# Optimization experiments

Measured on AMD Instinct MI355X. Metric: run time of the kernel, lower is better.

Reference implementation:

```python
import jax, jax.numpy as jnp
import numpy as np

D = 1024          # d_model
H = 16            # num_attention_heads
HD = D // H       # head_dim
WIN = 512         # attention_window (total)
W = WIN // 2      # one-sided window
S = 4096          # seq_len
B = 2             # batch
NEG = jnp.finfo(jnp.float32).min


def setup_inputs() -> dict:
    key = jax.random.key(0)
    ks = jax.random.split(key, 9)
    sc = 0.02
    return {
        "query": jax.random.normal(ks[0], (S, B, D), dtype=jnp.float32),
        "Wq": jax.random.normal(ks[1], (D, D), dtype=jnp.float32) * sc,
        "bq": jnp.zeros((D,), dtype=jnp.float32),
        "Wk": jax.random.normal(ks[2], (D, D), dtype=jnp.float32) * sc,
        "bk": jnp.zeros((D,), dtype=jnp.float32),
        "Wv": jax.random.normal(ks[3], (D, D), dtype=jnp.float32) * sc,
        "bv": jnp.zeros((D,), dtype=jnp.float32),
        "Wo": jax.random.normal(ks[4], (D, D), dtype=jnp.float32) * sc,
        "bo": jnp.zeros((D,), dtype=jnp.float32),
    }


def _heads(x):  # [B,S,D] -> [B,H,S,HD]
    b, s, _ = x.shape
    return x.reshape(b, s, H, HD).transpose(0, 2, 1, 3)


def reference(query, Wq, bq, Wk, bk, Wv, bv, Wo, bo):
    s, b, d = query.shape
    x = query.transpose(1, 0, 2)                       # [B,S,D]
    q = _heads(x @ Wq + bq) / jnp.sqrt(jnp.float32(HD))  # [B,H,S,HD]
    k = _heads(x @ Wk + bk)
    v = _heads(x @ Wv + bv)

    nc = s // W                                        # number of chunks
    # pad keys/values with one window of zeros on each side of seq axis
    kp = jnp.pad(k, ((0, 0), (0, 0), (W, W), (0, 0)))  # [B,H,S+2W,HD]
    vp = jnp.pad(v, ((0, 0), (0, 0), (W, W), (0, 0)))
    idx = jnp.arange(nc)[:, None] * W + jnp.arange(3 * W)[None, :]  # [nc,3W]
    kc = kp[:, :, idx]                                 # [B,H,nc,3W,HD]
    vc = vp[:, :, idx]
    qc = q.reshape(b, H, nc, W, HD)                    # [B,H,nc,W,HD]

    scores = jnp.einsum("bhcrd,bhckd->bhcrk", qc, kc)  # [B,H,nc,W,3W]

    r = jnp.arange(W)[:, None]                         # query offset in chunk
    kk = jnp.arange(3 * W)[None, :]
    band = (kk >= r) & (kk <= r + 2 * W)               # |kpos-qpos| <= W
    kpos = jnp.arange(nc)[:, None, None] * W + kk[None] - W   # [nc,1,3W] global key pos
    mask = band[None] & (kpos >= 0) & (kpos < s)       # [nc,W,3W]

    scores = jnp.where(mask[None, None], scores, NEG)
    probs = jax.nn.softmax(scores, axis=-1)
    out = jnp.einsum("bhcrk,bhckd->bhcrd", probs, vc)  # [B,H,nc,W,HD]
    out = out.reshape(b, H, s, HD).transpose(0, 2, 1, 3).reshape(b, s, d)
    out = out.transpose(1, 0, 2)                       # [S,B,D]
    return out @ Wo + bo
```

## Files before the change

### kernel.cpp

```cpp
#include <hip/hip_runtime.h>
#include <hip/hip_bf16.h>

#define SEQ 4096
#define BATCH 2
#define DMODEL 1024
#define NH 16
#define HDIM 64
#define NEGM (-1.0e30f)
#define NT 16

typedef __attribute__((ext_vector_type(8))) short bf16x8;
typedef __attribute__((ext_vector_type(8))) unsigned short us8;
typedef __attribute__((ext_vector_type(4))) unsigned short us4;
typedef __attribute__((ext_vector_type(4))) float f32x4;

__device__ __forceinline__ unsigned short f2bf(float f) {
    union { float f; unsigned u; } v; v.f = f;
    unsigned u = v.u;
    return (unsigned short)((u + 0x7fffu + ((u >> 16) & 1u)) >> 16);
}

#define GL16(g, l)                                                              \
    __builtin_amdgcn_global_load_lds(                                           \
        (const __attribute__((address_space(1))) unsigned int*)(g),             \
        (__attribute__((address_space(3))) unsigned int*)(l), 16, 0, 0)

__global__ __launch_bounds__(256) void transpose_w(const float* __restrict__ W,
                                                   unsigned short* __restrict__ Wt,
                                                   float scale) {
    __shared__ float tile[64][65];
    const int n0 = blockIdx.x * 64, k0 = blockIdx.y * 64;
    const int tx = threadIdx.x;
    for (int dy = threadIdx.y; dy < 64; dy += 4)
        tile[dy][tx] = W[(size_t)(k0 + dy) * DMODEL + n0 + tx];
    __syncthreads();
    for (int dy = threadIdx.y; dy < 64; dy += 4)
        Wt[(size_t)(n0 + dy) * DMODEL + k0 + tx] = f2bf(tile[tx][dy] * scale);
}

__global__ __launch_bounds__(256) void build_bcat(const float* __restrict__ bq,
                                                  const float* __restrict__ bk,
                                                  const float* __restrict__ bv,
                                                  float* __restrict__ bcat) {
    int i = blockIdx.x * 256 + threadIdx.x;
    float v;
    if (i < 1024) v = bq[i] * 0.125f;
    else if (i < 2048) v = bk[i - 1024];
    else v = bv[i - 2048];
    bcat[i] = v;
}

__global__ __launch_bounds__(256) void convert_x(const float* __restrict__ q,
                                                 unsigned short* __restrict__ xb) {
    int t = blockIdx.x * 256 + threadIdx.x;
    int d4 = (t & 255) * 4;
    int row = t >> 8;
    int b = row >> 12, s = row & (SEQ - 1);
    float4 v = *(const float4*)(q + ((size_t)s * BATCH + b) * DMODEL + d4);
    us4 o;
    o[0] = f2bf(v.x); o[1] = f2bf(v.y); o[2] = f2bf(v.z); o[3] = f2bf(v.w);
    *(us4*)(xb + (size_t)row * DMODEL + d4) = o;
}

__device__ __forceinline__ void store_qkv(float v0, float v1, float v2, float v3,
                                          int row0, int col, float bval,
                                          unsigned short* __restrict__ qb,
                                          unsigned short* __restrict__ kb,
                                          unsigned short* __restrict__ vtb) {
    const int proj = col >> 10;
    const int ch = col & 1023;
    const int h = ch >> 6, hd = ch & 63;
    float vv[4] = {v0, v1, v2, v3};
    if (proj == 2) {
        const int b = row0 >> 12, s = row0 & (SEQ - 1);
        us4 o;
#pragma unroll
        for (int r = 0; r < 4; ++r) o[r] = f2bf(vv[r] + bval);
        *(us4*)(vtb + ((size_t)(b * NH + h) * HDIM + hd) * SEQ + s) = o;
    } else {
        unsigned short* dst = (proj == 0) ? qb : kb;
#pragma unroll
        for (int r = 0; r < 4; ++r) {
            const int row = row0 + r;
            const int b = row >> 12, s = row & (SEQ - 1);
            dst[((size_t)(b * NH + h) * SEQ + s) * HDIM + hd] = f2bf(vv[r] + bval);
        }
    }
}

__global__ __launch_bounds__(512) void gemm192(const unsigned short* __restrict__ A,
                                               const unsigned short* __restrict__ Bt,
                                               const float* __restrict__ bias,
                                               unsigned short* __restrict__ qb,
                                               unsigned short* __restrict__ kb,
                                               unsigned short* __restrict__ vtb) {
    __shared__ __align__(16) unsigned short lds[57344];
    const int tid = threadIdx.x;
    const int lane = tid & 63, wid = tid >> 6;
    const int lr = lane & 15, lg = lane >> 4;
    const int wm = wid >> 2, wn = wid & 3;
    const int cpx = (int)gridDim.x >> 3;
    const int orig = ((int)blockIdx.x & 7) * cpx + ((int)blockIdx.x >> 3);
    const int m0 = (orig >> 4) * 256;
    const int n0 = (orig & 15) * 192;

    const int srow = wid * 8 + (lane >> 3);
    const int scol = ((lane & 7) ^ (lane >> 3)) << 3;

    f32x4 acc[8][3];
#pragma unroll
    for (int m = 0; m < 8; ++m)
#pragma unroll
        for (int n = 0; n < 3; ++n) {
            f32x4 z = {0.f, 0.f, 0.f, 0.f};
            acc[m][n] = z;
        }

    const unsigned short* gA = A + (size_t)(m0 + srow) * DMODEL + scol;
    const unsigned short* gB = Bt + (size_t)(n0 + srow) * DMODEL + scol;

#define STAGE192(kt, bsel)                                                       \
    do {                                                                         \
        const unsigned short* ga_ = gA + (kt) * 64;                              \
        unsigned short* la_ = &lds[(bsel) * 28672 + wid * 512];                  \
        _Pragma("unroll")                                                        \
        for (int r_ = 0; r_ < 4; ++r_)                                           \
            GL16(ga_ + (size_t)r_ * 64 * DMODEL, la_ + r_ * 4096);               \
        const unsigned short* gb_ = gB + (kt) * 64;                              \
        unsigned short* lb_ = &lds[(bsel) * 28672 + 16384 + wid * 512];          \
        _Pragma("unroll")                                                        \
        for (int r_ = 0; r_ < 3; ++r_)                                           \
            GL16(gb_ + (size_t)r_ * 64 * DMODEL, lb_ + r_ * 4096);               \
    } while (0)

    STAGE192(0, 0);
    asm volatile("s_waitcnt vmcnt(0)" ::: "memory");
    __builtin_amdgcn_s_barrier();
    asm volatile("" ::: "memory");

    const int swz = (lr & 7) << 3;
    for (int t = 0; t < NT; ++t) {
        if (t + 1 < NT) STAGE192(t + 1, (t + 1) & 1);
        const unsigned short* Ab = &lds[(t & 1) * 28672];
        const unsigned short* Bb = Ab + 16384;
#pragma unroll
        for (int ks = 0; ks < 2; ++ks) {
            const int kc = (ks * 32 + lg * 8) ^ swz;
            bf16x8 af[8], bfr[3];
#pragma unroll
            for (int fm = 0; fm < 8; ++fm)
                af[fm] = *(const bf16x8*)&Ab[(wm * 128 + fm * 16 + lr) * 64 + kc];
#pragma unroll
            for (int fn = 0; fn < 3; ++fn)
                bfr[fn] = *(const bf16x8*)&Bb[(wn * 48 + fn * 16 + lr) * 64 + kc];
            __builtin_amdgcn_s_setprio(1);
#pragma unroll
            for (int fm = 0; fm < 8; ++fm)
#pragma unroll
                for (int fn = 0; fn < 3; ++fn)
                    acc[fm][fn] = __builtin_amdgcn_mfma_f32_16x16x32_bf16(af[fm], bfr[fn], acc[fm][fn], 0, 0, 0);
            __builtin_amdgcn_s_setprio(0);
        }
        __builtin_amdgcn_sched_barrier(0);
        asm volatile("s_waitcnt lgkmcnt(0)" ::: "memory");
        asm volatile("s_waitcnt vmcnt(0)" ::: "memory");
        __builtin_amdgcn_s_barrier();
        asm volatile("" ::: "memory");
    }
#undef STAGE192

#pragma unroll
    for (int fn = 0; fn < 3; ++fn) {
        const int col = n0 + wn * 48 + fn * 16 + lr;
        const float bval = bias[col];
#pragma unroll
        for (int fm = 0; fm < 8; ++fm) {
            const int row0 = m0 + wm * 128 + fm * 16 + lg * 4;
            store_qkv(acc[fm][fn][0], acc[fm][fn][1], acc[fm][fn][2], acc[fm][fn][3],
                      row0, col, bval, qb, kb, vtb);
        }
    }
}

__global__ __launch_bounds__(512) void gemm256o(const unsigned short* __restrict__ A,
                                                const unsigned short* __restrict__ Bt,
                                                const float* __restrict__ bias,
                                                float* __restrict__ out) {
    __shared__ __align__(16) unsigned short lds[73728];
    const int tid = threadIdx.x;
    const int lane = tid & 63, wid = tid >> 6;
    const int lr = lane & 15, lg = lane >> 4;
    const int wm = wid >> 1, wn = wid & 1;
    const int cpx = (int)gridDim.x >> 3;
    const int orig = ((int)blockIdx.x & 7) * cpx + ((int)blockIdx.x >> 3);
    const int m0 = (orig >> 3) * 256;
    const int n0 = (orig & 7) * 128;

    const int srow = wid * 8 + (lane >> 3);
    const int scol = ((lane & 7) ^ (lane >> 3)) << 3;

    f32x4 acc[4][4];
#pragma unroll
    for (int m = 0; m < 4; ++m)
#pragma unroll
        for (int n = 0; n < 4; ++n) {
            f32x4 z = {0.f, 0.f, 0.f, 0.f};
            acc[m][n] = z;
        }

    const unsigned short* gA = A + (size_t)(m0 + srow) * DMODEL + scol;
    const unsigned short* gB = Bt + (size_t)(n0 + srow) * DMODEL + scol;

#define STAGE_A(kt, bsel)                                                        \
    do {                                                                         \
        const unsigned short* ga_ = gA + (kt) * 64;                              \
        unsigned short* la_ = &lds[(bsel) * 24576 + wid * 512];                  \
        _Pragma("unroll")                                                        \
        for (int r_ = 0; r_ < 4; ++r_)                                           \
            GL16(ga_ + (size_t)r_ * 64 * DMODEL, la_ + r_ * 4096);               \
    } while (0)
#define STAGE_B(kt, bsel)                                                        \
    do {                                                                         \
        const unsigned short* gb_ = gB + (kt) * 64;                              \
        unsigned short* lb_ = &lds[(bsel) * 24576 + 16384 + wid * 512];          \
        _Pragma("unroll")                                                        \
        for (int r_ = 0; r_ < 2; ++r_)                                           \
            GL16(gb_ + (size_t)r_ * 64 * DMODEL, lb_ + r_ * 4096);               \
    } while (0)

    STAGE_A(0, 0); STAGE_B(0, 0);
    STAGE_A(1, 1); STAGE_B(1, 1);
    asm volatile("s_waitcnt vmcnt(6)" ::: "memory");
    __builtin_amdgcn_s_barrier();
    asm volatile("" ::: "memory");

    const int swz = (lr & 7) << 3;
    int bs = 0;
    for (int t = 0; t < NT; ++t) {
        const int b2 = bs >= 1 ? bs - 1 : bs + 2;
        if (t + 2 < NT) { STAGE_A(t + 2, b2); STAGE_B(t + 2, b2); }
        const unsigned short* Ab = &lds[bs * 24576];
        const unsigned short* Bb = Ab + 16384;
#pragma unroll
        for (int ks = 0; ks < 2; ++ks) {
            const int kc = (ks * 32 + lg * 8) ^ swz;
            bf16x8 af[4], bfr[4];
#pragma unroll
            for (int fm = 0; fm < 4; ++fm)
                af[fm] = *(const bf16x8*)&Ab[(wm * 64 + fm * 16 + lr) * 64 + kc];
#pragma unroll
            for (int fn = 0; fn < 4; ++fn)
                bfr[fn] = *(const bf16x8*)&Bb[(wn * 64 + fn * 16 + lr) * 64 + kc];
            __builtin_amdgcn_s_setprio(1);
#pragma unroll
            for (int fm = 0; fm < 4; ++fm)
#pragma unroll
                for (int fn = 0; fn < 4; ++fn)
                    acc[fm][fn] = __builtin_amdgcn_mfma_f32_16x16x32_bf16(af[fm], bfr[fn], acc[fm][fn], 0, 0, 0);
            __builtin_amdgcn_s_setprio(0);
        }
        __builtin_amdgcn_sched_barrier(0);
        asm volatile("s_waitcnt lgkmcnt(0)" ::: "memory");
        if (t + 2 < NT)
            asm volatile("s_waitcnt vmcnt(6)" ::: "memory");
        else
            asm volatile("s_waitcnt vmcnt(0)" ::: "memory");
        __builtin_amdgcn_s_barrier();
        asm volatile("" ::: "memory");
        bs = bs < 2 ? bs + 1 : 0;
    }
#undef STAGE_A
#undef STAGE_B

#pragma unroll
    for (int fn = 0; fn < 4; ++fn) {
        const int col = n0 + wn * 64 + fn * 16 + lr;
        const float bval = bias[col];
#pragma unroll
        for (int fm = 0; fm < 4; ++fm) {
            const int row0 = m0 + wm * 64 + fm * 16 + lg * 4;
#pragma unroll
            for (int r = 0; r < 4; ++r) {
                const int row = row0 + r;
                const int b = row >> 12, s = row & (SEQ - 1);
                out[((size_t)s * BATCH + b) * DMODEL + col] = acc[fm][fn][r] + bval;
            }
        }
    }
}

__global__ __launch_bounds__(512) void attn_kernel(const unsigned short* __restrict__ qb,
                                                   const unsigned short* __restrict__ kb,
                                                   const unsigned short* __restrict__ vtb,
                                                   unsigned short* __restrict__ ao) {
    __shared__ __align__(16) unsigned short Ks[64][72];
    __shared__ __align__(16) unsigned short Vs[64][72];
    __shared__ __align__(16) unsigned short Ps[8][16][72];
    const int tid = threadIdx.x;
    const int lane = tid & 63, wid = tid >> 6;
    const int lr = lane & 15, lg = lane >> 4;
    const int blk = ((int)blockIdx.x & 7) * 128 + ((int)blockIdx.x >> 3);
    const int qc = blk & 31, h = (blk >> 5) & 15, b = blk >> 9;
    const int q0 = qc * 128;
    const unsigned short* Qh = qb + (size_t)(b * NH + h) * SEQ * HDIM;
    const unsigned short* Kh = kb + (size_t)(b * NH + h) * SEQ * HDIM;
    const unsigned short* Vh = vtb + (size_t)(b * NH + h) * HDIM * SEQ;
    const int qw = q0 + wid * 16;

    bf16x8 qf0 = *(const bf16x8*)(Qh + (size_t)(qw + lr) * HDIM + lg * 8);
    bf16x8 qf1 = *(const bf16x8*)(Qh + (size_t)(qw + lr) * HDIM + 32 + lg * 8);

    f32x4 oacc[4];
    float lsum[4];
#pragma unroll
    for (int n = 0; n < 4; ++n) {
        f32x4 z = {0.f, 0.f, 0.f, 0.f};
        oacc[n] = z;
    }
#pragma unroll
    for (int r = 0; r < 4; ++r) lsum[r] = 0.f;

    int lo = q0 - 256; if (lo < 0) lo = 0;
    int hi = q0 + 384; if (hi > SEQ) hi = SEQ;

    const int srow = tid >> 3, sseg = (tid & 7) * 8;

    us8 kpre = *(const us8*)(Kh + (size_t)(lo + srow) * HDIM + sseg);
    us8 vpre = *(const us8*)(Vh + (size_t)srow * SEQ + lo + sseg);

    for (int kt = lo; kt < hi; kt += 64) {
        __syncthreads();
        *(us8*)&Ks[srow][sseg] = kpre;
        *(us8*)&Vs[srow][sseg] = vpre;
        if (kt + 64 < hi) {
            kpre = *(const us8*)(Kh + (size_t)(kt + 64 + srow) * HDIM + sseg);
            vpre = *(const us8*)(Vh + (size_t)srow * SEQ + kt + 64 + sseg);
        }
        __builtin_amdgcn_sched_barrier(0);
        __syncthreads();

        f32x4 sf[4];
        __builtin_amdgcn_s_setprio(1);
#pragma unroll
        for (int n = 0; n < 4; ++n) {
            bf16x8 kf0 = *(const bf16x8*)&Ks[n * 16 + lr][lg * 8];
            bf16x8 kf1 = *(const bf16x8*)&Ks[n * 16 + lr][32 + lg * 8];
            f32x4 z = {0.f, 0.f, 0.f, 0.f};
            sf[n] = __builtin_amdgcn_mfma_f32_16x16x32_bf16(qf0, kf0, z, 0, 0, 0);
            sf[n] = __builtin_amdgcn_mfma_f32_16x16x32_bf16(qf1, kf1, sf[n], 0, 0, 0);
        }
        __builtin_amdgcn_s_setprio(0);
        const bool full = (kt >= qw - 241) && (kt + 63 <= qw + 256);
        if (!full) {
#pragma unroll
            for (int r = 0; r < 4; ++r) {
                const int qpos = qw + lg * 4 + r;
#pragma unroll
                for (int n = 0; n < 4; ++n) {
                    const int kpos = kt + n * 16 + lr;
                    if (kpos < qpos - 256 || kpos > qpos + 256) sf[n][r] = NEGM;
                }
            }
        }
#pragma unroll
        for (int n = 0; n < 4; ++n)
#pragma unroll
            for (int r = 0; r < 4; ++r) {
                const float p = __expf(sf[n][r]);
                lsum[r] += p;
                Ps[wid][lg * 4 + r][n * 16 + lr] = f2bf(p);
            }

        asm volatile("s_waitcnt lgkmcnt(0)" ::: "memory");
        __builtin_amdgcn_s_setprio(1);
#pragma unroll
        for (int ks = 0; ks < 2; ++ks) {
            bf16x8 pf = *(const bf16x8*)&Ps[wid][lr][ks * 32 + lg * 8];
#pragma unroll
            for (int n = 0; n < 4; ++n) {
                bf16x8 vf = *(const bf16x8*)&Vs[n * 16 + lr][ks * 32 + lg * 8];
                oacc[n] = __builtin_amdgcn_mfma_f32_16x16x32_bf16(pf, vf, oacc[n], 0, 0, 0);
            }
        }
        __builtin_amdgcn_s_setprio(0);
    }

#pragma unroll
    for (int d = 1; d < 16; d <<= 1)
#pragma unroll
        for (int r = 0; r < 4; ++r) lsum[r] += __shfl_xor(lsum[r], d, 64);

#pragma unroll
    for (int n = 0; n < 4; ++n)
#pragma unroll
        for (int r = 0; r < 4; ++r) {
            const int row = qw + lg * 4 + r;
            const float o = oacc[n][r] / lsum[r];
            ao[((size_t)b * SEQ + row) * DMODEL + h * HDIM + n * 16 + lr] = f2bf(o);
        }
}

extern "C" void kernel_launch(void* const* d_in, const int* in_sizes, int n_in,
                              void* d_out, int out_size, void* d_ws, size_t ws_size,
                              hipStream_t stream) {
    (void)in_sizes; (void)n_in; (void)out_size; (void)ws_size;
    const float* query = (const float*)d_in[0];
    const float* Wq = (const float*)d_in[1];
    const float* bq = (const float*)d_in[2];
    const float* Wk = (const float*)d_in[3];
    const float* bk = (const float*)d_in[4];
    const float* Wv = (const float*)d_in[5];
    const float* bv = (const float*)d_in[6];
    const float* Wo = (const float*)d_in[7];
    const float* bo = (const float*)d_in[8];
    float* out = (float*)d_out;

    char* ws = (char*)d_ws;
    unsigned short* xb   = (unsigned short*)ws;
    unsigned short* wcat = (unsigned short*)(ws + (16ull << 20));
    unsigned short* wot  = (unsigned short*)(ws + (22ull << 20));
    float*          bcat = (float*)(ws + (24ull << 20));
    unsigned short* qb   = (unsigned short*)(ws + (25ull << 20));
    unsigned short* kb   = (unsigned short*)(ws + (41ull << 20));
    unsigned short* vtb  = (unsigned short*)(ws + (57ull << 20));
    unsigned short* ao   = xb;

    transpose_w<<<dim3(16, 16), dim3(64, 4), 0, stream>>>(Wq, wcat, 0.125f);
    transpose_w<<<dim3(16, 16), dim3(64, 4), 0, stream>>>(Wk, wcat + 1024 * 1024, 1.0f);
    transpose_w<<<dim3(16, 16), dim3(64, 4), 0, stream>>>(Wv, wcat + 2 * 1024 * 1024, 1.0f);
    transpose_w<<<dim3(16, 16), dim3(64, 4), 0, stream>>>(Wo, wot, 1.0f);
    build_bcat<<<12, 256, 0, stream>>>(bq, bk, bv, bcat);
    convert_x<<<8192, 256, 0, stream>>>(query, xb);

    gemm192<<<512, 512, 0, stream>>>(xb, wcat, bcat, qb, kb, vtb);
    attn_kernel<<<1024, 512, 0, stream>>>(qb, kb, vtb, ao);
    gemm256o<<<256, 512, 0, stream>>>(ao, wot, bo, out);
}
```

Measured before the change: 169.1 us.

## Give each attention wave 32 query rows and halve the block size

The attention kernel now runs 4 waves of 256 threads, each handling two 16-row query groups instead of one. K and V fragments loaded from shared memory are reused across both groups, and each thread stages two rows of K/V per tile. This halves the LDS reads of K/V per query row and the number of waves that sync per tile. In exchange it needs more registers per wave for accumulators and has fewer waves per block to hide latency.

Result: slower. 178.8 us (+5.8%).

```diff
diff --git a/kernel.cpp b/kernel.cpp
--- a/kernel.cpp
+++ b/kernel.cpp
@@ -289,13 +289,13 @@
     }
 }
 
-__global__ __launch_bounds__(512) void attn_kernel(const unsigned short* __restrict__ qb,
+__global__ __launch_bounds__(256) void attn_kernel(const unsigned short* __restrict__ qb,
                                                    const unsigned short* __restrict__ kb,
                                                    const unsigned short* __restrict__ vtb,
                                                    unsigned short* __restrict__ ao) {
     __shared__ __align__(16) unsigned short Ks[64][72];
     __shared__ __align__(16) unsigned short Vs[64][72];
-    __shared__ __align__(16) unsigned short Ps[8][16][72];
+    __shared__ __align__(16) unsigned short Ps[4][32][72];
     const int tid = threadIdx.x;
     const int lane = tid & 63, wid = tid >> 6;
     const int lr = lane & 15, lg = lane >> 4;
@@ -305,81 +305,112 @@
     const unsigned short* Qh = qb + (size_t)(b * NH + h) * SEQ * HDIM;
     const unsigned short* Kh = kb + (size_t)(b * NH + h) * SEQ * HDIM;
     const unsigned short* Vh = vtb + (size_t)(b * NH + h) * HDIM * SEQ;
-    const int qw = q0 + wid * 16;
-
-    bf16x8 qf0 = *(const bf16x8*)(Qh + (size_t)(qw + lr) * HDIM + lg * 8);
-    bf16x8 qf1 = *(const bf16x8*)(Qh + (size_t)(qw + lr) * HDIM + 32 + lg * 8);
-
-    f32x4 oacc[4];
-    float lsum[4];
-#pragma unroll
-    for (int n = 0; n < 4; ++n) {
-        f32x4 z = {0.f, 0.f, 0.f, 0.f};
-        oacc[n] = z;
-    }
-#pragma unroll
-    for (int r = 0; r < 4; ++r) lsum[r] = 0.f;
+    const int qw = q0 + wid * 32;
+
+    bf16x8 qf[2][2];
+#pragma unroll
+    for (int g = 0; g < 2; ++g) {
+        qf[g][0] = *(const bf16x8*)(Qh + (size_t)(qw + g * 16 + lr) * HDIM + lg * 8);
+        qf[g][1] = *(const bf16x8*)(Qh + (size_t)(qw + g * 16 + lr) * HDIM + 32 + lg * 8);
+    }
+
+    f32x4 oacc[2][4];
+    float lsum[2][4];
+#pragma unroll
+    for (int g = 0; g < 2; ++g)
+#pragma unroll
+        for (int n = 0; n < 4; ++n) {
+            f32x4 z = {0.f, 0.f, 0.f, 0.f};
+            oacc[g][n] = z;
+        }
+#pragma unroll
+    for (int g = 0; g < 2; ++g)
+#pragma unroll
+        for (int r = 0; r < 4; ++r) lsum[g][r] = 0.f;
 
     int lo = q0 - 256; if (lo < 0) lo = 0;
     int hi = q0 + 384; if (hi > SEQ) hi = SEQ;
 
     const int srow = tid >> 3, sseg = (tid & 7) * 8;
 
-    us8 kpre = *(const us8*)(Kh + (size_t)(lo + srow) * HDIM + sseg);
-    us8 vpre = *(const us8*)(Vh + (size_t)srow * SEQ + lo + sseg);
+    us8 kpre0 = *(const us8*)(Kh + (size_t)(lo + srow) * HDIM + sseg);
+    us8 kpre1 = *(const us8*)(Kh + (size_t)(lo + srow + 32) * HDIM + sseg);
+    us8 vpre0 = *(const us8*)(Vh + (size_t)srow * SEQ + lo + sseg);
+    us8 vpre1 = *(const us8*)(Vh + (size_t)(srow + 32) * SEQ + lo + sseg);
 
     for (int kt = lo; kt < hi; kt += 64) {
         __syncthreads();
-        *(us8*)&Ks[srow][sseg] = kpre;
-        *(us8*)&Vs[srow][sseg] = vpre;
+        *(us8*)&Ks[srow][sseg]      = kpre0;
+        *(us8*)&Ks[srow + 32][sseg] = kpre1;
+        *(us8*)&Vs[srow][sseg]      = vpre0;
+        *(us8*)&Vs[srow + 32][sseg] = vpre1;
         if (kt + 64 < hi) {
-            kpre = *(const us8*)(Kh + (size_t)(kt + 64 + srow) * HDIM + sseg);
-            vpre = *(const us8*)(Vh + (size_t)srow * SEQ + kt + 64 + sseg);
+            kpre0 = *(const us8*)(Kh + (size_t)(kt + 64 + srow) * HDIM + sseg);
+            kpre1 = *(const us8*)(Kh + (size_t)(kt + 64 + srow + 32) * HDIM + sseg);
+            vpre0 = *(const us8*)(Vh + (size_t)srow * SEQ + kt + 64 + sseg);
+            vpre1 = *(const us8*)(Vh + (size_t)(srow + 32) * SEQ + kt + 64 + sseg);
         }
         __builtin_amdgcn_sched_barrier(0);
         __syncthreads();
 
-        f32x4 sf[4];
+        bf16x8 kf[4][2];
+#pragma unroll
+        for (int n = 0; n < 4; ++n) {
+            kf[n][0] = *(const bf16x8*)&Ks[n * 16 + lr][lg * 8];
+            kf[n][1] = *(const bf16x8*)&Ks[n * 16 + lr][32 + lg * 8];
+        }
+        f32x4 sf[2][4];
         __builtin_amdgcn_s_setprio(1);
 #pragma unroll
-        for (int n = 0; n < 4; ++n) {
-            bf16x8 kf0 = *(const bf16x8*)&Ks[n * 16 + lr][lg * 8];
-            bf16x8 kf1 = *(const bf16x8*)&Ks[n * 16 + lr][32 + lg * 8];
-            f32x4 z = {0.f, 0.f, 0.f, 0.f};
-            sf[n] = __builtin_amdgcn_mfma_f32_16x16x32_bf16(qf0, kf0, z, 0, 0, 0);
-            sf[n] = __builtin_amdgcn_mfma_f32_16x16x32_bf16(qf1, kf1, sf[n], 0, 0, 0);
-        }
+        for (int g = 0; g < 2; ++g)
+#pragma unroll
+            for (int n = 0; n < 4; ++n) {
+                f32x4 z = {0.f, 0.f, 0.f, 0.f};
+                sf[g][n] = __builtin_amdgcn_mfma_f32_16x16x32_bf16(qf[g][0], kf[n][0], z, 0, 0, 0);
+                sf[g][n] = __builtin_amdgcn_mfma_f32_16x16x32_bf16(qf[g][1], kf[n][1], sf[g][n], 0, 0, 0);
+            }
         __builtin_amdgcn_s_setprio(0);
-        const bool full = (kt >= qw - 241) && (kt + 63 <= qw + 256);
-        if (!full) {
-#pragma unroll
-            for (int r = 0; r < 4; ++r) {
-                const int qpos = qw + lg * 4 + r;
-#pragma unroll
-                for (int n = 0; n < 4; ++n) {
-                    const int kpos = kt + n * 16 + lr;
-                    if (kpos < qpos - 256 || kpos > qpos + 256) sf[n][r] = NEGM;
+#pragma unroll
+        for (int g = 0; g < 2; ++g) {
+            const int qwg = qw + g * 16;
+            const bool full = (kt >= qwg - 241) && (kt + 63 <= qwg + 256);
+            if (!full) {
+#pragma unroll
+                for (int r = 0; r < 4; ++r) {
+                    const int qpos = qwg + lg * 4 + r;
+#pragma unroll
+                    for (int n = 0; n < 4; ++n) {
+                        const int kpos = kt + n * 16 + lr;
+                        if (kpos < qpos - 256 || kpos > qpos + 256) sf[g][n][r] = NEGM;
+                    }
                 }
             }
         }
 #pragma unroll
-        for (int n = 0; n < 4; ++n)
-#pragma unroll
-            for (int r = 0; r < 4; ++r) {
-                const float p = __expf(sf[n][r]);
-                lsum[r] += p;
-                Ps[wid][lg * 4 + r][n * 16 + lr] = f2bf(p);
-            }
+        for (int g = 0; g < 2; ++g)
+#pragma unroll
+            for (int n = 0; n < 4; ++n)
+#pragma unroll
+                for (int r = 0; r < 4; ++r) {
+                    const float p = __expf(sf[g][n][r]);
+                    lsum[g][r] += p;
+                    Ps[wid][g * 16 + lg * 4 + r][n * 16 + lr] = f2bf(p);
+                }
 
         asm volatile("s_waitcnt lgkmcnt(0)" ::: "memory");
         __builtin_amdgcn_s_setprio(1);
 #pragma unroll
         for (int ks = 0; ks < 2; ++ks) {
-            bf16x8 pf = *(const bf16x8*)&Ps[wid][lr][ks * 32 + lg * 8];
-#pragma unroll
-            for (int n = 0; n < 4; ++n) {
-                bf16x8 vf = *(const bf16x8*)&Vs[n * 16 + lr][ks * 32 + lg * 8];
-                oacc[n] = __builtin_amdgcn_mfma_f32_16x16x32_bf16(pf, vf, oacc[n], 0, 0, 0);
+            bf16x8 vf[4];
+#pragma unroll
+            for (int n = 0; n < 4; ++n)
+                vf[n] = *(const bf16x8*)&Vs[n * 16 + lr][ks * 32 + lg * 8];
+#pragma unroll
+            for (int g = 0; g < 2; ++g) {
+                bf16x8 pf = *(const bf16x8*)&Ps[wid][g * 16 + lr][ks * 32 + lg * 8];
+#pragma unroll
+                for (int n = 0; n < 4; ++n)
+                    oacc[g][n] = __builtin_amdgcn_mfma_f32_16x16x32_bf16(pf, vf[n], oacc[g][n], 0, 0, 0);
             }
         }
         __builtin_amdgcn_s_setprio(0);
@@ -388,16 +419,20 @@
 #pragma unroll
     for (int d = 1; d < 16; d <<= 1)
 #pragma unroll
-        for (int r = 0; r < 4; ++r) lsum[r] += __shfl_xor(lsum[r], d, 64);
-
-#pragma unroll
-    for (int n = 0; n < 4; ++n)
-#pragma unroll
-        for (int r = 0; r < 4; ++r) {
-            const int row = qw + lg * 4 + r;
-            const float o = oacc[n][r] / lsum[r];
-            ao[((size_t)b * SEQ + row) * DMODEL + h * HDIM + n * 16 + lr] = f2bf(o);
-        }
+        for (int g = 0; g < 2; ++g)
+#pragma unroll
+            for (int r = 0; r < 4; ++r) lsum[g][r] += __shfl_xor(lsum[g][r], d, 64);
+
+#pragma unroll
+    for (int g = 0; g < 2; ++g)
+#pragma unroll
+        for (int n = 0; n < 4; ++n)
+#pragma unroll
+            for (int r = 0; r < 4; ++r) {
+                const int row = qw + g * 16 + lg * 4 + r;
+                const float o = oacc[g][n][r] / lsum[g][r];
+                ao[((size_t)b * SEQ + row) * DMODEL + h * HDIM + n * 16 + lr] = f2bf(o);
+            }
 }
 
 extern "C" void kernel_launch(void* const* d_in, const int* in_sizes, int n_in,
@@ -433,6 +468,6 @@
     convert_x<<<8192, 256, 0, stream>>>(query, xb);
 
     gemm192<<<512, 512, 0, stream>>>(xb, wcat, bcat, qb, kb, vtb);
-    attn_kernel<<<1024, 512, 0, stream>>>(qb, kb, vtb, ao);
+    attn_kernel<<<1024, 256, 0, stream>>>(qb, kb, vtb, ao);
     gemm256o<<<256, 512, 0, stream>>>(ao, wot, bo, out);
 }
```
